# Kernel optimization log

Hardware: AMD Instinct MI355X
Metric: run time of the kernel (lower is better)

## Reference

```python
import math
import jax, jax.numpy as jnp
import numpy as np

FACTOR = 3  # AutoCorrelation(factor=3)

def reference(queries, keys, values):
    # queries/keys/values: [B, L, D]; source requires L == S for the broadcast below.
    B, L, D = queries.shape
    S = keys.shape[1]
    # NOTE (faithful to source): rfft is over the LAST axis with fft_length L/S,
    # i.e. the feature axis D is zero-padded (or truncated) to length L.
    q_fft = jnp.fft.rfft(queries, n=L, axis=-1)          # [B, L, L//2+1] complex
    k_fft = jnp.fft.rfft(keys, n=S, axis=-1)             # [B, S, S//2+1] complex
    corr = jnp.fft.irfft(q_fft * jnp.conj(k_fft), n=L + S - 1, axis=-1)  # [B, L, L+S-1]

    top_k = int(FACTOR * math.log(float(L)))
    mean_value = jnp.mean(corr, axis=1)                  # [B, L+S-1]
    top_k = min(top_k, mean_value.shape[-1])
    top_k_val, top_k_ind = jax.lax.top_k(mean_value, top_k)  # [B, K]
    tmp_corr = jax.nn.softmax(top_k_val, axis=-1)        # [B, K]

    # Faithful to source: the roll shift for every batch element uses the
    # delays of batch element 0 (index[0] in the TF loop).
    shifts = top_k_ind[0]                                # [K] int32
    # Vectorized replacement of the per-index tf.roll loop.
    V_rolled = jax.vmap(lambda s: jnp.roll(values, -s, axis=1))(shifts)  # [K, B, L, D]
    # Weighted aggregation over the K retained delays (intended semantics of
    # the source einsum, which as written has a rank mismatch).
    output = jnp.einsum('kbld,bk->bld', V_rolled, tmp_corr)  # [B, L, D]
    return output

def setup_inputs() -> dict:
    key = jax.random.key(0)
    k1, k2, k3 = jax.random.split(key, 3)
    B, L, D = 8, 1024, 512
    return {
        'queries': jax.random.normal(k1, (B, L, D), dtype=jnp.float32),
        'keys':    jax.random.normal(k2, (B, L, D), dtype=jnp.float32),
        'values':  jax.random.normal(k3, (B, L, D), dtype=jnp.float32),
    }
```

## Files before the change

### kernel.cpp

```cpp
#include <hip/hip_runtime.h>
#include <math.h>

#define NB 8
#define NL 1024
#define ND 512
#define NF 513
#define NT 2047
#define TOPK 20

typedef __attribute__((ext_vector_type(8))) short short8;
typedef __attribute__((ext_vector_type(4))) float f32x4;

static __device__ __forceinline__ unsigned short bf16_rne(float x) {
    unsigned int u = __builtin_bit_cast(unsigned int, x);
    unsigned int r = (u + 0x7fffu + ((u >> 16) & 1u)) >> 16;
    return (unsigned short)r;
}
static __device__ __forceinline__ float bf16_to_f(unsigned short h) {
    unsigned int u = ((unsigned int)h) << 16;
    return __builtin_bit_cast(float, u);
}

__global__ __launch_bounds__(256) void k_tr(const float* __restrict__ q,
                                            const float* __restrict__ kk,
                                            unsigned short* __restrict__ Thi,
                                            unsigned short* __restrict__ Tlo) {
    __shared__ float tile[64][65];
    const int which = blockIdx.z;
    const int b  = blockIdx.y;
    const int l0 = (blockIdx.x & 15) * 64;
    const int d0 = (blockIdx.x >> 4) * 64;
    const float* src = (which ? kk : q) + (size_t)b * NL * ND;
    const int t = threadIdx.x;
    const int r = t >> 4, c = t & 15;
    #pragma unroll
    for (int rr = 0; rr < 4; ++rr) {
        const float4 v = *(const float4*)&src[(size_t)(l0 + r + 16 * rr) * ND + d0 + c * 4];
        tile[r + 16 * rr][c * 4 + 0] = v.x;
        tile[r + 16 * rr][c * 4 + 1] = v.y;
        tile[r + 16 * rr][c * 4 + 2] = v.z;
        tile[r + 16 * rr][c * 4 + 3] = v.w;
    }
    __syncthreads();
    unsigned short* hi = Thi + ((size_t)which * NB + b) * (size_t)ND * NL;
    unsigned short* lo = Tlo + ((size_t)which * NB + b) * (size_t)ND * NL;
    #pragma unroll
    for (int p = 0; p < 2; ++p) {
        const int c2 = t + 256 * p;
        const int dl = c2 >> 3;
        const int l8 = (c2 & 7) * 8;
        short8 vh, vl;
        #pragma unroll
        for (int i = 0; i < 8; ++i) {
            const float x = tile[l8 + i][dl];
            const unsigned short h = bf16_rne(x);
            vh[i] = (short)h;
            vl[i] = (short)bf16_rne(x - bf16_to_f(h));
        }
        *(short8*)&hi[(size_t)(d0 + dl) * NL + l0 + l8] = vh;
        *(short8*)&lo[(size_t)(d0 + dl) * NL + l0 + l8] = vl;
    }
}

#define GBK 64
#define GPAD 8

__global__ __launch_bounds__(256, 1) void k_gemm(const unsigned short* __restrict__ Thi,
                                                 const unsigned short* __restrict__ Tlo,
                                                 float* __restrict__ S) {
    __shared__ unsigned short Ahi[128][GBK + GPAD];
    __shared__ unsigned short Alo[128][GBK + GPAD];
    __shared__ unsigned short Bhi[128][GBK + GPAD];
    __shared__ unsigned short Blo[128][GBK + GPAD];
    __shared__ float sd[255];
    const int b  = blockIdx.z >> 1;
    const int kh = blockIdx.z & 1;
    const int mt = blockIdx.x, nt = blockIdx.y;
    const int tid  = threadIdx.x;
    const int lane = tid & 63, w = tid >> 6;
    const int wr = w >> 1, wc = w & 1;
    const int m = lane & 15, g = lane >> 4;

    const size_t plane = (size_t)ND * NL;
    const unsigned short* qhi = Thi + (size_t)b * plane;
    const unsigned short* khi = Thi + ((size_t)NB + b) * plane;
    const unsigned short* qlo = Tlo + (size_t)b * plane;
    const unsigned short* klo = Tlo + ((size_t)NB + b) * plane;

    f32x4 acc[4][4];
    #pragma unroll
    for (int i = 0; i < 4; ++i)
        #pragma unroll
        for (int j = 0; j < 4; ++j) acc[i][j] = (f32x4)(0.f);

    for (int kt = kh * 8; kt < kh * 8 + 8; ++kt) {
        __syncthreads();
        #pragma unroll
        for (int p = 0; p < 4; ++p) {
            const int cc  = tid + 256 * p;
            const int row = cc >> 3, col8 = (cc & 7) * 8;
            const size_t ga = (size_t)(mt * 128 + row) * NL + kt * GBK + col8;
            const size_t gb = (size_t)(nt * 128 + row) * NL + kt * GBK + col8;
            *(short8*)&Ahi[row][col8] = *(const short8*)&qhi[ga];
            *(short8*)&Alo[row][col8] = *(const short8*)&qlo[ga];
            *(short8*)&Bhi[row][col8] = *(const short8*)&khi[gb];
            *(short8*)&Blo[row][col8] = *(const short8*)&klo[gb];
        }
        __syncthreads();
        #pragma unroll
        for (int ks = 0; ks < 2; ++ks) {
            short8 ah[4], al[4], bh[4], bl[4];
            #pragma unroll
            for (int i = 0; i < 4; ++i) {
                ah[i] = *(const short8*)&Ahi[wr * 64 + i * 16 + m][ks * 32 + g * 8];
                al[i] = *(const short8*)&Alo[wr * 64 + i * 16 + m][ks * 32 + g * 8];
            }
            #pragma unroll
            for (int j = 0; j < 4; ++j) {
                bh[j] = *(const short8*)&Bhi[wc * 64 + j * 16 + m][ks * 32 + g * 8];
                bl[j] = *(const short8*)&Blo[wc * 64 + j * 16 + m][ks * 32 + g * 8];
            }
            #pragma unroll
            for (int i = 0; i < 4; ++i)
                #pragma unroll
                for (int j = 0; j < 4; ++j) {
                    acc[i][j] = __builtin_amdgcn_mfma_f32_16x16x32_bf16(ah[i], bh[j], acc[i][j], 0, 0, 0);
                    acc[i][j] = __builtin_amdgcn_mfma_f32_16x16x32_bf16(ah[i], bl[j], acc[i][j], 0, 0, 0);
                    acc[i][j] = __builtin_amdgcn_mfma_f32_16x16x32_bf16(al[i], bh[j], acc[i][j], 0, 0, 0);
                }
        }
    }

    if (tid < 255) sd[tid] = 0.f;
    __syncthreads();
    float bin[7][4];
    #pragma unroll
    for (int u = 0; u < 7; ++u)
        #pragma unroll
        for (int r2 = 0; r2 < 4; ++r2) bin[u][r2] = 0.f;
    #pragma unroll
    for (int i = 0; i < 4; ++i)
        #pragma unroll
        for (int j = 0; j < 4; ++j)
            #pragma unroll
            for (int r2 = 0; r2 < 4; ++r2) bin[i - j + 3][r2] += acc[i][j][r2];
    const int basei = (wr - wc) * 64 + g * 4 - m + 127;
    #pragma unroll
    for (int u = 0; u < 7; ++u)
        #pragma unroll
        for (int r2 = 0; r2 < 4; ++r2)
            atomicAdd(&sd[basei + (u - 3) * 16 + r2], bin[u][r2]);
    __syncthreads();
    const int doff = (mt - nt) * 128 + 511 - 127;
    if (tid < 255) atomicAdd(&S[b * 1023 + doff + tid], sd[tid]);
}

__global__ __launch_bounds__(64) void k_pdft(const float* __restrict__ S,
                                             float* __restrict__ pbar) {
    const int b = blockIdx.y;
    const int f = blockIdx.x;
    const int lane = threadIdx.x;
    const float w = 2.0f * 3.14159265358979323846f / 1024.0f;
    float re = 0.f, im = 0.f;
    #pragma unroll
    for (int i = 0; i < 16; ++i) {
        const int j = lane + 64 * i;
        if (j < 1023) {
            const int mm = (f * (j - 511)) & 1023;
            float s, c;
            sincosf(w * (float)mm, &s, &c);
            const float x = S[b * 1023 + j];
            re = fmaf(x, c, re);
            im = fmaf(x, -s, im);
        }
    }
    #pragma unroll
    for (int off = 32; off; off >>= 1) {
        re += __shfl_xor(re, off);
        im += __shfl_xor(im, off);
    }
    if (lane == 0) {
        pbar[b * 2 * NF + 2 * f]     = re;
        pbar[b * 2 * NF + 2 * f + 1] = im;
    }
}

__global__ __launch_bounds__(256) void k_mean(const float* __restrict__ pbar,
                                              float* __restrict__ mv) {
    __shared__ float P[2 * NF];
    const int b = blockIdx.y;
    for (int i = threadIdx.x; i < 2 * NF; i += 256)
        P[i] = pbar[(size_t)b * (2 * NF) + i];
    __syncthreads();
    const int wave = threadIdx.x >> 6, lane = threadIdx.x & 63;
    const int t = blockIdx.x * 4 + wave;
    if (t >= NT) return;
    const float w2 = 2.0f * 3.14159265358979323846f / 2047.0f;
    float acc = 0.f;
    #pragma unroll
    for (int i = 0; i < 8; ++i) {
        const int f = 1 + lane + 64 * i;
        const int mm = (f * t) % 2047;
        float s, c;
        sincosf(w2 * (float)mm, &s, &c);
        acc = fmaf(P[2 * f], c, acc);
        acc = fmaf(-P[2 * f + 1], s, acc);
    }
    acc *= 2.0f;
    #pragma unroll
    for (int off = 32; off; off >>= 1) acc += __shfl_xor(acc, off);
    if (lane == 0)
        mv[(size_t)b * NT + t] = (acc + P[0]) * (1.0f / (2047.0f * 1024.0f));
}

__global__ __launch_bounds__(64) void k_topk(const float* __restrict__ mv,
                                             float* __restrict__ wts,
                                             int* __restrict__ shifts) {
    __shared__ float v[NT];
    __shared__ float topv[TOPK];
    __shared__ int   topi[TOPK];
    const int b = blockIdx.x;
    const int t = threadIdx.x;
    for (int i = t; i < NT; i += 64) v[i] = mv[(size_t)b * NT + i];
    __syncthreads();
    for (int kkk = 0; kkk < TOPK; ++kkk) {
        float bv = -INFINITY; int bi = 0x7fffffff;
        for (int i = t; i < NT; i += 64) {
            float x = v[i];
            if (x > bv) { bv = x; bi = i; }
        }
        #pragma unroll
        for (int off = 32; off; off >>= 1) {
            float ov = __shfl_down(bv, off);
            int   oi = __shfl_down(bi, off);
            if (ov > bv || (ov == bv && oi < bi)) { bv = ov; bi = oi; }
        }
        bv = __shfl(bv, 0); bi = __shfl(bi, 0);
        if (t == 0) { topv[kkk] = bv; topi[kkk] = bi; }
        v[bi] = -INFINITY;
        __syncthreads();
    }
    if (t == 0) {
        float m = topv[0], sum = 0.f, e[TOPK];
        #pragma unroll
        for (int i = 0; i < TOPK; ++i) { e[i] = expf(topv[i] - m); sum += e[i]; }
        #pragma unroll
        for (int i = 0; i < TOPK; ++i) wts[b * TOPK + i] = e[i] / sum;
        if (b == 0) {
            #pragma unroll
            for (int i = 0; i < TOPK; ++i) shifts[i] = topi[i];
        }
    }
}

__global__ __launch_bounds__(128) void k_out(const float* __restrict__ vals,
                                             const float* __restrict__ wts,
                                             const int* __restrict__ shifts,
                                             float* __restrict__ out) {
    __shared__ float w[TOPK];
    __shared__ int   sh[TOPK];
    const int id = blockIdx.x;
    const int b = id & 7;
    const int l = id >> 3;
    const int t = threadIdx.x;
    if (t < TOPK) { w[t] = wts[b * TOPK + t]; sh[t] = shifts[t]; }
    __syncthreads();
    float4 acc = make_float4(0.f, 0.f, 0.f, 0.f);
    const float4* vb = (const float4*)(vals + (size_t)b * NL * ND);
    #pragma unroll 4
    for (int kkk = 0; kkk < TOPK; ++kkk) {
        const int sl = (l + sh[kkk]) & (NL - 1);
        const float4 x = vb[(size_t)sl * (ND / 4) + t];
        const float wk = w[kkk];
        acc.x = fmaf(wk, x.x, acc.x);
        acc.y = fmaf(wk, x.y, acc.y);
        acc.z = fmaf(wk, x.z, acc.z);
        acc.w = fmaf(wk, x.w, acc.w);
    }
    ((float4*)out)[((size_t)b * NL + l) * (ND / 4) + t] = acc;
}

extern "C" void kernel_launch(void* const* d_in, const int* in_sizes, int n_in,
                              void* d_out, int out_size, void* d_ws, size_t ws_size,
                              hipStream_t stream) {
    const float* q = (const float*)d_in[0];
    const float* k = (const float*)d_in[1];
    const float* v = (const float*)d_in[2];
    float* out    = (float*)d_out;

    const size_t plane = (size_t)ND * NL;
    unsigned short* Thi = (unsigned short*)d_ws;
    unsigned short* Tlo = Thi + 2 * NB * plane;
    float* S      = (float*)(Tlo + 2 * NB * plane);
    float* pbar   = S + NB * 1023;
    float* mv     = pbar + NB * 2 * NF;
    float* wts    = mv + NB * NT;
    int*   shifts = (int*)(wts + NB * TOPK);

    hipMemsetAsync(S, 0, NB * 1023 * sizeof(float), stream);
    k_tr  <<<dim3(128, NB, 2), 256, 0, stream>>>(q, k, Thi, Tlo);
    k_gemm<<<dim3(4, 4, NB * 2), 256, 0, stream>>>(Thi, Tlo, S);
    k_pdft<<<dim3(NF, NB), 64, 0, stream>>>(S, pbar);
    k_mean<<<dim3(512, NB), 256, 0, stream>>>(pbar, mv);
    k_topk<<<NB, 64, 0, stream>>>(mv, wts, shifts);
    k_out <<<NL * NB, 128, 0, stream>>>(v, wts, shifts, out);
}
```

Before: 220.7 us.

## Split GEMM reduction four ways, prefetch tiles via registers, widen top-k block

```diff
diff --git a/kernel.cpp b/kernel.cpp
--- a/kernel.cpp
+++ b/kernel.cpp
@@ -64,18 +64,20 @@
 
 #define GBK 64
 #define GPAD 8
-
-__global__ __launch_bounds__(256, 1) void k_gemm(const unsigned short* __restrict__ Thi,
+#define GKT 4
+
+__global__ __launch_bounds__(256, 2) void k_gemm(const unsigned short* __restrict__ Thi,
                                                  const unsigned short* __restrict__ Tlo,
                                                  float* __restrict__ S) {
     __shared__ unsigned short Ahi[128][GBK + GPAD];
     __shared__ unsigned short Alo[128][GBK + GPAD];
     __shared__ unsigned short Bhi[128][GBK + GPAD];
     __shared__ unsigned short Blo[128][GBK + GPAD];
-    __shared__ float sd[255];
-    const int b  = blockIdx.z >> 1;
-    const int kh = blockIdx.z & 1;
-    const int mt = blockIdx.x, nt = blockIdx.y;
+    __shared__ float sd4[4][256];
+    const int id   = blockIdx.x;
+    const int b    = id & 7;
+    const int rest = id >> 3;
+    const int mt = rest & 3, nt = (rest >> 2) & 3, kq = rest >> 4;
     const int tid  = threadIdx.x;
     const int lane = tid & 63, w = tid >> 6;
     const int wr = w >> 1, wc = w & 1;
@@ -93,20 +95,45 @@
         #pragma unroll
         for (int j = 0; j < 4; ++j) acc[i][j] = (f32x4)(0.f);
 
-    for (int kt = kh * 8; kt < kh * 8 + 8; ++kt) {
+    const int kbase = kq * GKT;
+    short8 r_ah[4], r_al[4], r_bh[4], r_bl[4];
+    #pragma unroll
+    for (int p = 0; p < 4; ++p) {
+        const int cc  = tid + 256 * p;
+        const int row = cc >> 3, col8 = (cc & 7) * 8;
+        const size_t ga = (size_t)(mt * 128 + row) * NL + kbase * GBK + col8;
+        const size_t gb = (size_t)(nt * 128 + row) * NL + kbase * GBK + col8;
+        r_ah[p] = *(const short8*)&qhi[ga];
+        r_al[p] = *(const short8*)&qlo[ga];
+        r_bh[p] = *(const short8*)&khi[gb];
+        r_bl[p] = *(const short8*)&klo[gb];
+    }
+
+    for (int kt = 0; kt < GKT; ++kt) {
         __syncthreads();
         #pragma unroll
         for (int p = 0; p < 4; ++p) {
             const int cc  = tid + 256 * p;
             const int row = cc >> 3, col8 = (cc & 7) * 8;
-            const size_t ga = (size_t)(mt * 128 + row) * NL + kt * GBK + col8;
-            const size_t gb = (size_t)(nt * 128 + row) * NL + kt * GBK + col8;
-            *(short8*)&Ahi[row][col8] = *(const short8*)&qhi[ga];
-            *(short8*)&Alo[row][col8] = *(const short8*)&qlo[ga];
-            *(short8*)&Bhi[row][col8] = *(const short8*)&khi[gb];
-            *(short8*)&Blo[row][col8] = *(const short8*)&klo[gb];
+            *(short8*)&Ahi[row][col8] = r_ah[p];
+            *(short8*)&Alo[row][col8] = r_al[p];
+            *(short8*)&Bhi[row][col8] = r_bh[p];
+            *(short8*)&Blo[row][col8] = r_bl[p];
         }
         __syncthreads();
+        if (kt + 1 < GKT) {
+            #pragma unroll
+            for (int p = 0; p < 4; ++p) {
+                const int cc  = tid + 256 * p;
+                const int row = cc >> 3, col8 = (cc & 7) * 8;
+                const size_t ga = (size_t)(mt * 128 + row) * NL + (kbase + kt + 1) * GBK + col8;
+                const size_t gb = (size_t)(nt * 128 + row) * NL + (kbase + kt + 1) * GBK + col8;
+                r_ah[p] = *(const short8*)&qhi[ga];
+                r_al[p] = *(const short8*)&qlo[ga];
+                r_bh[p] = *(const short8*)&khi[gb];
+                r_bl[p] = *(const short8*)&klo[gb];
+            }
+        }
         #pragma unroll
         for (int ks = 0; ks < 2; ++ks) {
             short8 ah[4], al[4], bh[4], bl[4];
@@ -131,7 +158,7 @@
         }
     }
 
-    if (tid < 255) sd[tid] = 0.f;
+    for (int i = tid; i < 1024; i += 256) ((float*)sd4)[i] = 0.f;
     __syncthreads();
     float bin[7][4];
     #pragma unroll
@@ -149,10 +176,13 @@
     for (int u = 0; u < 7; ++u)
         #pragma unroll
         for (int r2 = 0; r2 < 4; ++r2)
-            atomicAdd(&sd[basei + (u - 3) * 16 + r2], bin[u][r2]);
+            atomicAdd(&sd4[w][basei + (u - 3) * 16 + r2], bin[u][r2]);
     __syncthreads();
     const int doff = (mt - nt) * 128 + 511 - 127;
-    if (tid < 255) atomicAdd(&S[b * 1023 + doff + tid], sd[tid]);
+    if (tid < 255) {
+        const float vsum = sd4[0][tid] + sd4[1][tid] + sd4[2][tid] + sd4[3][tid];
+        atomicAdd(&S[b * 1023 + doff + tid], vsum);
+    }
 }
 
 __global__ __launch_bounds__(64) void k_pdft(const float* __restrict__ S,
@@ -213,31 +243,45 @@
         mv[(size_t)b * NT + t] = (acc + P[0]) * (1.0f / (2047.0f * 1024.0f));
 }
 
-__global__ __launch_bounds__(64) void k_topk(const float* __restrict__ mv,
-                                             float* __restrict__ wts,
-                                             int* __restrict__ shifts) {
+__global__ __launch_bounds__(256) void k_topk(const float* __restrict__ mv,
+                                              float* __restrict__ wts,
+                                              int* __restrict__ shifts) {
     __shared__ float v[NT];
     __shared__ float topv[TOPK];
     __shared__ int   topi[TOPK];
+    __shared__ float wv[4];
+    __shared__ int   wi[4];
     const int b = blockIdx.x;
     const int t = threadIdx.x;
-    for (int i = t; i < NT; i += 64) v[i] = mv[(size_t)b * NT + i];
+    const int lane = t & 63, wave = t >> 6;
+    for (int i = t; i < NT; i += 256) v[i] = mv[(size_t)b * NT + i];
     __syncthreads();
     for (int kkk = 0; kkk < TOPK; ++kkk) {
         float bv = -INFINITY; int bi = 0x7fffffff;
-        for (int i = t; i < NT; i += 64) {
-            float x = v[i];
-            if (x > bv) { bv = x; bi = i; }
+        #pragma unroll
+        for (int s = 0; s < 8; ++s) {
+            const int i = t + 256 * s;
+            if (i < NT) {
+                const float x = v[i];
+                if (x > bv) { bv = x; bi = i; }
+            }
         }
         #pragma unroll
         for (int off = 32; off; off >>= 1) {
-            float ov = __shfl_down(bv, off);
-            int   oi = __shfl_down(bi, off);
+            const float ov = __shfl_down(bv, off);
+            const int   oi = __shfl_down(bi, off);
             if (ov > bv || (ov == bv && oi < bi)) { bv = ov; bi = oi; }
         }
-        bv = __shfl(bv, 0); bi = __shfl(bi, 0);
-        if (t == 0) { topv[kkk] = bv; topi[kkk] = bi; }
-        v[bi] = -INFINITY;
+        if (lane == 0) { wv[wave] = bv; wi[wave] = bi; }
+        __syncthreads();
+        if (t == 0) {
+            bv = wv[0]; bi = wi[0];
+            #pragma unroll
+            for (int ww = 1; ww < 4; ++ww)
+                if (wv[ww] > bv || (wv[ww] == bv && wi[ww] < bi)) { bv = wv[ww]; bi = wi[ww]; }
+            topv[kkk] = bv; topi[kkk] = bi;
+            v[bi] = -INFINITY;
+        }
         __syncthreads();
     }
     if (t == 0) {
@@ -299,9 +343,9 @@
 
     hipMemsetAsync(S, 0, NB * 1023 * sizeof(float), stream);
     k_tr  <<<dim3(128, NB, 2), 256, 0, stream>>>(q, k, Thi, Tlo);
-    k_gemm<<<dim3(4, 4, NB * 2), 256, 0, stream>>>(Thi, Tlo, S);
+    k_gemm<<<512, 256, 0, stream>>>(Thi, Tlo, S);
     k_pdft<<<dim3(NF, NB), 64, 0, stream>>>(S, pbar);
     k_mean<<<dim3(512, NB), 256, 0, stream>>>(pbar, mv);
-    k_topk<<<NB, 64, 0, stream>>>(mv, wts, shifts);
+    k_topk<<<NB, 256, 0, stream>>>(mv, wts, shifts);
     k_out <<<NL * NB, 128, 0, stream>>>(v, wts, shifts, out);
 }
```

Result: faster. 185.2 us (-16.1%).
